# Performance work log

Hardware: AMD Instinct MI355X
Metric: run time of the kernel (lower is better)

## Reference

```python
import jax, jax.numpy as jnp
import numpy as np

HEAD, D_MODEL, D_KV = 16, 1024, 64
B, NQ, NK = 2, 2048, 2048


def setup_inputs() -> dict:
    key = jax.random.key(0)
    ks = jax.random.split(key, 10)
    s = 1.0 / np.sqrt(D_MODEL)
    return {
        "queries": jax.random.normal(ks[0], (B, NQ, D_MODEL), jnp.float32),
        "keys": jax.random.normal(ks[1], (B, NK, D_MODEL), jnp.float32),
        "values": jax.random.normal(ks[2], (B, NK, D_MODEL), jnp.float32),
        "group_prob": jax.random.uniform(ks[3], (B, 1, NQ, NK), jnp.float32),
        "attention_mask": jnp.ones((B, NK), jnp.int32),
        "Wq": jax.random.normal(ks[4], (D_MODEL, HEAD * D_KV), jnp.float32) * s,
        "bq": jnp.zeros((HEAD * D_KV,), jnp.float32),
        "Wk": jax.random.normal(ks[5], (D_MODEL, HEAD * D_KV), jnp.float32) * s,
        "bk": jnp.zeros((HEAD * D_KV,), jnp.float32),
        "Wv": jax.random.normal(ks[6], (D_MODEL, HEAD * D_KV), jnp.float32) * s,
        "bv": jnp.zeros((HEAD * D_KV,), jnp.float32),
    }


def reference(queries, keys, values, group_prob, attention_mask, Wq, bq, Wk, bk, Wv, bv):
    b_s, nq, _ = queries.shape
    nk = keys.shape[1]
    # projections -> [b, h, n, d]
    q = (queries @ Wq + bq).reshape(b_s, nq, HEAD, D_KV).transpose(0, 2, 1, 3)
    k = (keys @ Wk + bk).reshape(b_s, nk, HEAD, D_KV).transpose(0, 2, 1, 3)
    v = (values @ Wv + bv).reshape(b_s, nk, HEAD, D_KV).transpose(0, 2, 1, 3)
    att = jnp.einsum("bhqd,bhkd->bhqk", q, k) / np.sqrt(D_KV).astype(np.float32)
    # NOTE: original uses non-in-place `att.masked_fill(...)` and discards the
    # result, so attention_mask has NO effect on the computation. Replicated.
    att = jax.nn.softmax(att, axis=-1)
    att = att * group_prob  # post-softmax group gating, broadcast over heads
    out = jnp.einsum("bhqk,bhkd->bhqd", att, v)
    return out.transpose(0, 2, 1, 3).reshape(b_s, nq, D_MODEL)
```

## Files before the change

kernel.cpp:

```cpp
#include <hip/hip_runtime.h>
#include <hip/hip_bf16.h>
#include <cstdint>

typedef unsigned short ushort_t;
typedef __attribute__((ext_vector_type(8))) short short8;
typedef __attribute__((ext_vector_type(4))) short short4v;
typedef __attribute__((ext_vector_type(4))) float floatx4;
typedef __attribute__((ext_vector_type(4))) unsigned int uintx4;
typedef __attribute__((ext_vector_type(4))) unsigned short ushort4_t;

#define H_   16
#define DKV_ 64
#define DM_  1024
#define B_   2
#define NQ_  2048
#define NK_  2048

__device__ __forceinline__ unsigned short f2bf(float f) {
  union { float f; unsigned int u; } v; v.f = f;
  unsigned int u = v.u;
  return (unsigned short)((u + 0x7fffu + ((u >> 16) & 1u)) >> 16);
}

__device__ __forceinline__ float fexp2(float x) { return __builtin_amdgcn_exp2f(x); }
__device__ __forceinline__ float frcp(float x)  { return __builtin_amdgcn_rcpf(x); }

__device__ __forceinline__ unsigned int cvt_pk_bf16(float lo, float hi) {
  unsigned int r;
  asm("v_cvt_pk_bf16_f32 %0, %1, %2" : "=v"(r) : "v"(lo), "v"(hi));
  return r;
}

__device__ __forceinline__ floatx4 mfma16(short8 a, short8 b, floatx4 c) {
  return __builtin_amdgcn_mfma_f32_16x16x32_bf16(a, b, c, 0, 0, 0);
}

__device__ __forceinline__ void gload_lds16(const ushort_t* g, ushort_t* l) {
  __builtin_amdgcn_global_load_lds(
      (const __attribute__((address_space(1))) void*)g,
      (__attribute__((address_space(3))) void*)l, 16, 0, 0);
}

__global__ __launch_bounds__(256) void cast_x_kernel(
    const float* __restrict__ q, const float* __restrict__ k,
    const float* __restrict__ v, ushort_t* __restrict__ dst)
{
  const int t = blockIdx.y;
  const float* src = (t == 0) ? q : (t == 1) ? k : v;
  ushort_t* d = dst + (size_t)t * 4096 * 1024;
  const int gid = blockIdx.x * 256 + threadIdx.x;
  #pragma unroll
  for (int u = 0; u < 8; u++) {
    const int i4 = u * 131072 + gid;
    floatx4 f = ((const floatx4*)src)[i4];
    ushort4_t o;
    #pragma unroll
    for (int e = 0; e < 4; e++) o[e] = f2bf(f[e]);
    *(ushort4_t*)&d[(size_t)i4 * 4] = o;
  }
}

__global__ __launch_bounds__(256) void cast_wt_kernel(
    const float* __restrict__ Wq, const float* __restrict__ Wk,
    const float* __restrict__ Wv, ushort_t* __restrict__ WtAll)
{
  __shared__ ushort_t tile[32][33];
  const int t = blockIdx.z;
  const float* W = (t == 0) ? Wq : (t == 1) ? Wk : Wv;
  ushort_t* Wt = WtAll + (size_t)t * 1024 * 1024;
  const int n0 = blockIdx.x * 32, k0 = blockIdx.y * 32;
  const int tid = threadIdx.x, r = tid >> 3, c4 = (tid & 7) * 4;
  floatx4 f = *(const floatx4*)&W[(size_t)(k0 + r) * 1024 + n0 + c4];
  #pragma unroll
  for (int e = 0; e < 4; e++) tile[r][c4 + e] = f2bf(f[e]);
  __syncthreads();
  ushort4_t o;
  #pragma unroll
  for (int e = 0; e < 4; e++) o[e] = tile[c4 + e][r];
  *(ushort4_t*)&Wt[(size_t)(n0 + r) * 1024 + k0 + c4] = o;
}

__global__ __launch_bounds__(256, 2) void proj_kernel2(
    const ushort_t* __restrict__ Xbf, const ushort_t* __restrict__ WtAll,
    const float* __restrict__ bq, const float* __restrict__ bk,
    const float* __restrict__ bv,
    ushort_t* __restrict__ Qb, ushort_t* __restrict__ Kb, ushort_t* __restrict__ Vt)
{
  const int mode = blockIdx.z;
  const ushort_t* X  = Xbf  + (size_t)mode * 4096 * 1024;
  const ushort_t* Wt = WtAll + (size_t)mode * 1024 * 1024;
  const float* bias  = (mode == 0) ? bq : (mode == 1) ? bk : bv;
  ushort_t* dst      = (mode == 0) ? Qb : (mode == 1) ? Kb : Vt;

  __shared__ ushort_t SM[8192];
  ushort_t* SA = SM;
  ushort_t* SB = SM + 4096;

  const int tid = threadIdx.x, lane = tid & 63, wid = tid >> 6;
  const int c = lane & 15, g = lane >> 4;
  const int m0 = blockIdx.y * 128, n0 = blockIdx.x * 128;
  const int wm = wid & 1, wn = wid >> 1, mb = wm * 64, nb = wn * 64;
  const int srow = lane >> 2;
  const int schunk = (lane & 3) * 8;

  floatx4 acc[4][4];
  #pragma unroll
  for (int i = 0; i < 4; i++)
    #pragma unroll
    for (int j = 0; j < 4; j++) acc[i][j] = floatx4{0.f, 0.f, 0.f, 0.f};

  for (int k0 = 0; k0 < DM_; k0 += 32) {
    __syncthreads();
    #pragma unroll
    for (int u = 0; u < 2; u++) {
      const int t = wid * 2 + u;
      gload_lds16(&X [(size_t)(m0 + t * 16 + srow) * 1024 + k0 + schunk], &SA[t * 512]);
      gload_lds16(&Wt[(size_t)(n0 + t * 16 + srow) * 1024 + k0 + schunk], &SB[t * 512]);
    }
    __syncthreads();

    short8 af[4], bfr[4];
    #pragma unroll
    for (int i = 0; i < 4; i++) af[i]  = *(const short8*)&SA[(mb + i * 16 + c) * 32 + g * 8];
    #pragma unroll
    for (int j = 0; j < 4; j++) bfr[j] = *(const short8*)&SB[(nb + j * 16 + c) * 32 + g * 8];
    #pragma unroll
    for (int i = 0; i < 4; i++)
      #pragma unroll
      for (int j = 0; j < 4; j++) acc[i][j] = mfma16(af[i], bfr[j], acc[i][j]);
  }

  __syncthreads();
  const float scale = (mode == 0) ? 0.18033688011112042f : 1.0f;
  ushort_t* EP = SM + wid * 2048;
  const int hh = (n0 + nb) >> 6;

  if (mode != 2) {
    for (int jj = 0; jj < 2; jj++) {
      #pragma unroll
      for (int jt = 0; jt < 2; jt++) {
        const int j = jj * 2 + jt;
        const float bb = bias[n0 + nb + j * 16 + c];
        #pragma unroll
        for (int i = 0; i < 4; i++)
          #pragma unroll
          for (int r = 0; r < 4; r++)
            EP[(i * 16 + g * 4 + r) * 32 + jt * 16 + c] =
                f2bf((acc[i][j][r] + bb) * scale);
      }
      #pragma unroll
      for (int u = 0; u < 8; u++) {
        const int rowl = u * 8 + (lane >> 3);
        ushort4_t vv = *(ushort4_t*)&EP[rowl * 32 + (lane & 7) * 4];
        const int rowg = m0 + mb + rowl;
        const int bb2 = rowg >> 11, nn = rowg & 2047;
        *(ushort4_t*)&dst[((size_t)(bb2 * H_ + hh) * NQ_ + nn) * DKV_ +
                          jj * 32 + (lane & 7) * 4] = vv;
      }
    }
  } else {
    const int bb2 = (m0 + mb) >> 11, nloc = (m0 + mb) & 2047;
    for (int j = 0; j < 4; j++) {
      const float bb = bias[n0 + nb + j * 16 + c];
      #pragma unroll
      for (int i = 0; i < 4; i++) {
        ushort4_t pk;
        #pragma unroll
        for (int r = 0; r < 4; r++) pk[r] = f2bf(acc[i][j][r] + bb);
        *(ushort4_t*)&EP[c * 72 + i * 16 + g * 4] = pk;
      }
      const int d0 = j * 16;
      #pragma unroll
      for (int u = 0; u < 2; u++) {
        const int coll = u * 8 + (lane >> 3);
        short8 vv = *(const short8*)&EP[coll * 72 + (lane & 7) * 8];
        *(short8*)&dst[((size_t)(bb2 * H_ + hh) * DKV_ + d0 + coll) * NK_ +
                       nloc + (lane & 7) * 8] = vv;
      }
    }
  }
}

constexpr int LDT = 40;
__global__ __launch_bounds__(256, 2) void proj_kernel_fb(
    const float* __restrict__ Xq, const float* __restrict__ Xk, const float* __restrict__ Xv,
    const float* __restrict__ Wq, const float* __restrict__ Wk, const float* __restrict__ Wv,
    const float* __restrict__ bq, const float* __restrict__ bk, const float* __restrict__ bv,
    ushort_t* __restrict__ Qb, ushort_t* __restrict__ Kb, ushort_t* __restrict__ Vt)
{
  const int mode = blockIdx.z;
  const float* X    = (mode == 0) ? Xq : (mode == 1) ? Xk : Xv;
  const float* W    = (mode == 0) ? Wq : (mode == 1) ? Wk : Wv;
  const float* bias = (mode == 0) ? bq : (mode == 1) ? bk : bv;
  ushort_t* dst     = (mode == 0) ? Qb : (mode == 1) ? Kb : Vt;

  __shared__ ushort_t Asm[128 * LDT];
  __shared__ ushort_t Bsm[128 * LDT];

  const int tid = threadIdx.x, lane = tid & 63, wid = tid >> 6;
  const int m0 = blockIdx.y * 128, n0 = blockIdx.x * 128;
  const int c = lane & 15, g = lane >> 4;
  const int wm = wid & 1, wn = wid >> 1, mb = wm * 64, nb = wn * 64;

  floatx4 acc[4][4];
  #pragma unroll
  for (int i = 0; i < 4; i++)
    #pragma unroll
    for (int j = 0; j < 4; j++) acc[i][j] = floatx4{0.f, 0.f, 0.f, 0.f};

  const int ar = tid >> 1, ah = tid & 1;
  const int bn = tid & 127, bh2 = tid >> 7;

  for (int k0 = 0; k0 < DM_; k0 += 32) {
    const floatx4* ap = (const floatx4*)(X + (size_t)(m0 + ar) * DM_ + k0 + ah * 16);
    floatx4 av0 = ap[0], av1 = ap[1], av2 = ap[2], av3 = ap[3];
    const float* wp = W + (size_t)(k0 + bh2 * 16) * 1024 + n0 + bn;
    float wv[16];
    #pragma unroll
    for (int j = 0; j < 16; j++) wv[j] = wp[j * 1024];
    short8 pa0, pa1, pb0, pb1;
    #pragma unroll
    for (int j = 0; j < 4; j++) {
      pa0[j] = (short)f2bf(av0[j]); pa0[4 + j] = (short)f2bf(av1[j]);
      pa1[j] = (short)f2bf(av2[j]); pa1[4 + j] = (short)f2bf(av3[j]);
    }
    #pragma unroll
    for (int j = 0; j < 8; j++) { pb0[j] = (short)f2bf(wv[j]); pb1[j] = (short)f2bf(wv[8 + j]); }
    __syncthreads();
    *(short8*)&Asm[ar * LDT + ah * 16]      = pa0;
    *(short8*)&Asm[ar * LDT + ah * 16 + 8]  = pa1;
    *(short8*)&Bsm[bn * LDT + bh2 * 16]     = pb0;
    *(short8*)&Bsm[bn * LDT + bh2 * 16 + 8] = pb1;
    __syncthreads();
    short8 af[4], bfr[4];
    #pragma unroll
    for (int i = 0; i < 4; i++) af[i]  = *(const short8*)&Asm[(mb + i * 16 + c) * LDT + g * 8];
    #pragma unroll
    for (int j = 0; j < 4; j++) bfr[j] = *(const short8*)&Bsm[(nb + j * 16 + c) * LDT + g * 8];
    #pragma unroll
    for (int i = 0; i < 4; i++)
      #pragma unroll
      for (int j = 0; j < 4; j++) acc[i][j] = mfma16(af[i], bfr[j], acc[i][j]);
  }
  #pragma unroll
  for (int j = 0; j < 4; j++) {
    const int col = n0 + nb + j * 16 + c;
    const float bv_ = bias[col];
    const int h = col >> 6, d = col & 63;
    #pragma unroll
    for (int i = 0; i < 4; i++)
      #pragma unroll
      for (int r = 0; r < 4; r++) {
        const int row = m0 + mb + i * 16 + g * 4 + r;
        const int b = row >> 11, n = row & 2047;
        float v = acc[i][j][r] + bv_;
        if (mode == 0) {
          v *= 0.18033688011112042f;
          dst[((size_t)(b * H_ + h) * NQ_ + n) * DKV_ + d] = f2bf(v);
        } else if (mode == 1) {
          dst[((size_t)(b * H_ + h) * NQ_ + n) * DKV_ + d] = f2bf(v);
        } else {
          dst[((size_t)(b * H_ + h) * DKV_ + d) * NK_ + n] = f2bf(v);
        }
      }
  }
}

__global__ __launch_bounds__(512, 4) void attn_kernel(
    const ushort_t* __restrict__ Qb, const ushort_t* __restrict__ Kb,
    const ushort_t* __restrict__ Vt, const float* __restrict__ gp,
    float* __restrict__ out)
{
  __shared__ ushort_t Ks[2][64 * 72];
  __shared__ ushort_t Vs[2][64 * 72];

  constexpr int NT = NK_ / 64;

  const int tid = threadIdx.x, lane = tid & 63, wid = tid >> 6;
  const int c = lane & 15, g = lane >> 4;
  const int h = blockIdx.x, b = blockIdx.z;
  const int bh = b * H_ + h;
  const int qw = blockIdx.y * 128 + wid * 16;

  const ushort_t* Qp = Qb + (size_t)bh * NQ_ * DKV_;
  const ushort_t* Kp = Kb + (size_t)bh * NK_ * DKV_;
  const ushort_t* Vp = Vt + (size_t)bh * DKV_ * NK_;
  const float* gpq = gp + (size_t)b * NQ_ * NK_ + (size_t)(qw + c) * NK_;

  const int srow = tid >> 3;
  const int u    = tid & 7;
  const int scol = u * 8;
  const int so_lo = 32 * (u >> 2) + 8 * ((2 * u) & 3) + 4 * ((u >> 1) & 1);
  const int so_hi = 32 * (u >> 2) + 8 * ((2 * u + 1) & 3) + 4 * ((u >> 1) & 1);

  short8 qf[2];
  #pragma unroll
  for (int kc = 0; kc < 2; kc++)
    qf[kc] = *(const short8*)&Qp[(qw + c) * DKV_ + kc * 32 + g * 8];

  *(short8*)&Ks[0][srow * 72 + scol] = *(const short8*)&Kp[(size_t)srow * DKV_ + scol];
  {
    short8 v8 = *(const short8*)&Vp[(size_t)srow * NK_ + scol];
    short4v vl, vh;
    #pragma unroll
    for (int e = 0; e < 4; e++) { vl[e] = v8[e]; vh[e] = v8[4 + e]; }
    *(short4v*)&Vs[0][srow * 72 + so_lo] = vl;
    *(short4v*)&Vs[0][srow * 72 + so_hi] = vh;
  }
  short8 kA = *(const short8*)&Kp[(size_t)(64 + srow) * DKV_ + scol];
  short8 vA = *(const short8*)&Vp[(size_t)srow * NK_ + 64 + scol];
  short8 kB = {}, vB = {};
  floatx4 gpA[4], gpB[4];
  #pragma unroll
  for (int jk = 0; jk < 4; jk++)
    gpA[jk] = *(const floatx4*)&gpq[jk * 16 + g * 4];
  __syncthreads();

  floatx4 o[4];
  float l = 0.f;
  #pragma unroll
  for (int jd = 0; jd < 4; jd++) o[jd] = floatx4{0.f, 0.f, 0.f, 0.f};

#define ATTN_BODY(T, CUR, GPC, GPN, KA, VA, KB, VB)                          \
  {                                                                          \
    const int t_ = (T);                                                      \
            \
    if (t_ + 2 < NT) {                                                       \
      const int k2 = (t_ + 2) * 64;                                          \
      KB = *(const short8*)&Kp[(size_t)(k2 + srow) * DKV_ + scol];           \
      VB = *(const short8*)&Vp[(size_t)srow * NK_ + k2 + scol];              \
    }                                                                        \
                                     \
    if (t_ + 1 < NT) {                                                       \
      const int k1 = (t_ + 1) * 64;                                          \
      _Pragma("unroll")                                                      \
      for (int jk = 0; jk < 4; jk++)                                         \
        GPN[jk] = *(const floatx4*)&gpq[k1 + jk * 16 + g * 4];               \
    }                                                                        \
                  \
    floatx4 s_[4];                                                           \
    _Pragma("unroll")                                                        \
    for (int jk = 0; jk < 4; jk++) {                                         \
      s_[jk] = floatx4{0.f, 0.f, 0.f, 0.f};                                  \
      _Pragma("unroll")                                                      \
      for (int kc = 0; kc < 2; kc++) {                                       \
        short8 kf = *(const short8*)&Ks[CUR][(jk * 16 + c) * 72 + kc * 32 + g * 8]; \
        s_[jk] = mfma16(kf, qf[kc], s_[jk]);                                 \
      }                                                                      \
    }                                                                        \
              \
    uintx4 afw_[2];                                                          \
    _Pragma("unroll")                                                        \
    for (int jk = 0; jk < 4; jk++) {                                         \
      const float p0 = fexp2(s_[jk][0]);                                     \
      const float p1 = fexp2(s_[jk][1]);                                     \
      const float p2 = fexp2(s_[jk][2]);                                     \
      const float p3 = fexp2(s_[jk][3]);                                     \
      l += (p0 + p1) + (p2 + p3);                                            \
      const unsigned int w0 = cvt_pk_bf16(p0 * GPC[jk][0], p1 * GPC[jk][1]); \
      const unsigned int w1 = cvt_pk_bf16(p2 * GPC[jk][2], p3 * GPC[jk][3]); \
      afw_[jk >> 1][2 * (jk & 1) + 0] = w0;                                  \
      afw_[jk >> 1][2 * (jk & 1) + 1] = w1;                                  \
    }                                                                        \
             \
    _Pragma("unroll")                                                        \
    for (int kc = 0; kc < 2; kc++) {                                         \
      const short8 af_ = __builtin_bit_cast(short8, afw_[kc]);               \
      _Pragma("unroll")                                                      \
      for (int jd = 0; jd < 4; jd++) {                                       \
        short8 vf = *(const short8*)&Vs[CUR][(jd * 16 + c) * 72 + kc * 32 + g * 8]; \
        o[jd] = mfma16(af_, vf, o[jd]);                                      \
      }                                                                      \
    }                                                                        \
              \
    if (t_ + 1 < NT) {                                                       \
      *(short8*)&Ks[(CUR) ^ 1][srow * 72 + scol] = KA;                       \
      short4v vl_, vh_;                                                      \
      _Pragma("unroll")                                                      \
      for (int e = 0; e < 4; e++) { vl_[e] = VA[e]; vh_[e] = VA[4 + e]; }    \
      *(short4v*)&Vs[(CUR) ^ 1][srow * 72 + so_lo] = vl_;                    \
      *(short4v*)&Vs[(CUR) ^ 1][srow * 72 + so_hi] = vh_;                    \
    }                                                                        \
    __syncthreads();                                                         \
  }

  for (int tt = 0; tt < NT; tt += 2) {
    ATTN_BODY(tt,     0, gpA, gpB, kA, vA, kB, vB)
    ATTN_BODY(tt + 1, 1, gpB, gpA, kB, vB, kA, vA)
  }
#undef ATTN_BODY

  float lf = l;
  lf += __shfl_xor(lf, 16);
  lf += __shfl_xor(lf, 32);
  const float inv = frcp(lf);
  float invr[4];
  #pragma unroll
  for (int r = 0; r < 4; r++) invr[r] = __shfl(inv, g * 4 + r);

  #pragma unroll
  for (int jd = 0; jd < 4; jd++)
    #pragma unroll
    for (int r = 0; r < 4; r++) {
      const int row = qw + g * 4 + r;
      out[(size_t)(b * NQ_ + row) * 1024 + h * 64 + jd * 16 + c] =
          o[jd][r] * invr[r];
    }
}

extern "C" void kernel_launch(void* const* d_in, const int* in_sizes, int n_in,
                              void* d_out, int out_size, void* d_ws, size_t ws_size,
                              hipStream_t stream) {
  const float* queries = (const float*)d_in[0];
  const float* keys    = (const float*)d_in[1];
  const float* values  = (const float*)d_in[2];
  const float* gp      = (const float*)d_in[3];
  const float* Wq = (const float*)d_in[5];
  const float* bq = (const float*)d_in[6];
  const float* Wk = (const float*)d_in[7];
  const float* bk = (const float*)d_in[8];
  const float* Wv = (const float*)d_in[9];
  const float* bv = (const float*)d_in[10];

  const size_t SZ_QKV = (size_t)3 * B_ * H_ * NQ_ * DKV_;
  const size_t SZ_X   = (size_t)3 * 4096 * 1024;
  const size_t SZ_W   = (size_t)3 * 1024 * 1024;
  const size_t NEED   = (SZ_QKV + SZ_X + SZ_W) * sizeof(ushort_t);

  ushort_t* Qb = (ushort_t*)d_ws;
  ushort_t* Kb = Qb + (size_t)B_ * H_ * NQ_ * DKV_;
  ushort_t* Vt = Kb + (size_t)B_ * H_ * NK_ * DKV_;
  float* out = (float*)d_out;

  if (ws_size >= NEED) {
    ushort_t* Xbf = Qb + SZ_QKV;
    ushort_t* Wt  = Xbf + SZ_X;
    cast_x_kernel<<<dim3(512, 3), 256, 0, stream>>>(queries, keys, values, Xbf);
    cast_wt_kernel<<<dim3(32, 32, 3), 256, 0, stream>>>(Wq, Wk, Wv, Wt);
    proj_kernel2<<<dim3(8, 32, 3), 256, 0, stream>>>(
        Xbf, Wt, bq, bk, bv, Qb, Kb, Vt);
  } else {
    proj_kernel_fb<<<dim3(8, 32, 3), 256, 0, stream>>>(
        queries, keys, values, Wq, Wk, Wv, bq, bk, bv, Qb, Kb, Vt);
  }
  attn_kernel<<<dim3(H_, NQ_ / 128, B_), 512, 0, stream>>>(Qb, Kb, Vt, gp, out);
}
```

Baseline: 256.2 us.

## Read K/V fragments directly from global memory, drop LDS staging and barriers

The attention kernel no longer stages K and V tiles through shared memory with double buffering and __syncthreads. Each wave instead loads its MFMA fragments straight from global memory, relying on L2/cache reuse across the waves of a block. The projection kernels now write V in the pre-permuted column order the attention loop expects. The change also remaps block indices so heads sharing an XCD are grouped, and adds s_setprio around the MFMA sections. This removes LDS traffic and barrier stalls, but adds global-load latency and redundant loads across waves that must be hidden by occupancy.

```diff
diff --git a/kernel.cpp b/kernel.cpp
--- a/kernel.cpp
+++ b/kernel.cpp
@@ -160,6 +160,9 @@
     }
   } else {
     const int bb2 = (m0 + mb) >> 11, nloc = (m0 + mb) & 2047;
+    const int u2 = lane & 7;
+    const int slo = 32 * (u2 >> 2) + 8 * ((2 * u2) & 3) + 4 * ((u2 >> 1) & 1);
+    const int shi = 32 * (u2 >> 2) + 8 * ((2 * u2 + 1) & 3) + 4 * ((u2 >> 1) & 1);
     for (int j = 0; j < 4; j++) {
       const float bb = bias[n0 + nb + j * 16 + c];
       #pragma unroll
@@ -173,9 +176,13 @@
       #pragma unroll
       for (int u = 0; u < 2; u++) {
         const int coll = u * 8 + (lane >> 3);
-        short8 vv = *(const short8*)&EP[coll * 72 + (lane & 7) * 8];
-        *(short8*)&dst[((size_t)(bb2 * H_ + hh) * DKV_ + d0 + coll) * NK_ +
-                       nloc + (lane & 7) * 8] = vv;
+        short8 vv = *(const short8*)&EP[coll * 72 + u2 * 8];
+        short4v vl, vh;
+        #pragma unroll
+        for (int e = 0; e < 4; e++) { vl[e] = vv[e]; vh[e] = vv[4 + e]; }
+        ushort_t* base = &dst[((size_t)(bb2 * H_ + hh) * DKV_ + d0 + coll) * NK_ + nloc];
+        *(short4v*)&base[slo] = vl;
+        *(short4v*)&base[shi] = vh;
       }
     }
   }
@@ -260,7 +267,11 @@
         } else if (mode == 1) {
           dst[((size_t)(b * H_ + h) * NQ_ + n) * DKV_ + d] = f2bf(v);
         } else {
-          dst[((size_t)(b * H_ + h) * DKV_ + d) * NK_ + n] = f2bf(v);
+          const int tb = n & ~63, w = n & 63, u2 = w >> 3, e = w & 7;
+          const int slo = 32 * (u2 >> 2) + 8 * ((2 * u2) & 3) + 4 * ((u2 >> 1) & 1);
+          const int shi = 32 * (u2 >> 2) + 8 * ((2 * u2 + 1) & 3) + 4 * ((u2 >> 1) & 1);
+          const int phys = tb + (e < 4 ? slo + e : shi + e - 4);
+          dst[((size_t)(b * H_ + h) * DKV_ + d) * NK_ + phys] = f2bf(v);
         }
       }
   }
@@ -271,83 +282,63 @@
     const ushort_t* __restrict__ Vt, const float* __restrict__ gp,
     float* __restrict__ out)
 {
-  __shared__ ushort_t Ks[2][64 * 72];
-  __shared__ ushort_t Vs[2][64 * 72];
-
   constexpr int NT = NK_ / 64;
 
   const int tid = threadIdx.x, lane = tid & 63, wid = tid >> 6;
   const int c = lane & 15, g = lane >> 4;
-  const int h = blockIdx.x, b = blockIdx.z;
-  const int bh = b * H_ + h;
-  const int qw = blockIdx.y * 128 + wid * 16;
+
+  const int flat = blockIdx.x + (blockIdx.y << 4) + (blockIdx.z << 8);
+  const int xcd = flat & 7, i = flat >> 3;
+  const int qy = i & 15;
+  const int bh = xcd + ((i >> 4) << 3);
+  const int b = bh >> 4, h = bh & 15;
+
+  const int qw = qy * 128 + wid * 16;
 
   const ushort_t* Qp = Qb + (size_t)bh * NQ_ * DKV_;
   const ushort_t* Kp = Kb + (size_t)bh * NK_ * DKV_;
   const ushort_t* Vp = Vt + (size_t)bh * DKV_ * NK_;
   const float* gpq = gp + (size_t)b * NQ_ * NK_ + (size_t)(qw + c) * NK_;
 
-  const int srow = tid >> 3;
-  const int u    = tid & 7;
-  const int scol = u * 8;
-  const int so_lo = 32 * (u >> 2) + 8 * ((2 * u) & 3) + 4 * ((u >> 1) & 1);
-  const int so_hi = 32 * (u >> 2) + 8 * ((2 * u + 1) & 3) + 4 * ((u >> 1) & 1);
-
   short8 qf[2];
   #pragma unroll
   for (int kc = 0; kc < 2; kc++)
     qf[kc] = *(const short8*)&Qp[(qw + c) * DKV_ + kc * 32 + g * 8];
 
-  *(short8*)&Ks[0][srow * 72 + scol] = *(const short8*)&Kp[(size_t)srow * DKV_ + scol];
-  {
-    short8 v8 = *(const short8*)&Vp[(size_t)srow * NK_ + scol];
-    short4v vl, vh;
-    #pragma unroll
-    for (int e = 0; e < 4; e++) { vl[e] = v8[e]; vh[e] = v8[4 + e]; }
-    *(short4v*)&Vs[0][srow * 72 + so_lo] = vl;
-    *(short4v*)&Vs[0][srow * 72 + so_hi] = vh;
-  }
-  short8 kA = *(const short8*)&Kp[(size_t)(64 + srow) * DKV_ + scol];
-  short8 vA = *(const short8*)&Vp[(size_t)srow * NK_ + 64 + scol];
-  short8 kB = {}, vB = {};
+  floatx4 o[4];
+  float l = 0.f;
+  #pragma unroll
+  for (int jd = 0; jd < 4; jd++) o[jd] = floatx4{0.f, 0.f, 0.f, 0.f};
+
   floatx4 gpA[4], gpB[4];
   #pragma unroll
   for (int jk = 0; jk < 4; jk++)
     gpA[jk] = *(const floatx4*)&gpq[jk * 16 + g * 4];
-  __syncthreads();
-
-  floatx4 o[4];
-  float l = 0.f;
-  #pragma unroll
-  for (int jd = 0; jd < 4; jd++) o[jd] = floatx4{0.f, 0.f, 0.f, 0.f};
-
-#define ATTN_BODY(T, CUR, GPC, GPN, KA, VA, KB, VB)                          \
+
+#define ATTN_BODY(T, GPC, GPN)                                               \
   {                                                                          \
     const int t_ = (T);                                                      \
-            \
-    if (t_ + 2 < NT) {                                                       \
-      const int k2 = (t_ + 2) * 64;                                          \
-      KB = *(const short8*)&Kp[(size_t)(k2 + srow) * DKV_ + scol];           \
-      VB = *(const short8*)&Vp[(size_t)srow * NK_ + k2 + scol];              \
-    }                                                                        \
-                                     \
+    const int k0 = t_ * 64;                                                  \
     if (t_ + 1 < NT) {                                                       \
-      const int k1 = (t_ + 1) * 64;                                          \
+      const int k1 = k0 + 64;                                                \
       _Pragma("unroll")                                                      \
       for (int jk = 0; jk < 4; jk++)                                         \
         GPN[jk] = *(const floatx4*)&gpq[k1 + jk * 16 + g * 4];               \
     }                                                                        \
                   \
     floatx4 s_[4];                                                           \
+    __builtin_amdgcn_s_setprio(1);                                           \
     _Pragma("unroll")                                                        \
     for (int jk = 0; jk < 4; jk++) {                                         \
       s_[jk] = floatx4{0.f, 0.f, 0.f, 0.f};                                  \
       _Pragma("unroll")                                                      \
       for (int kc = 0; kc < 2; kc++) {                                       \
-        short8 kf = *(const short8*)&Ks[CUR][(jk * 16 + c) * 72 + kc * 32 + g * 8]; \
+        short8 kf = *(const short8*)&Kp[(size_t)(k0 + jk * 16 + c) * DKV_ +  \
+                                        kc * 32 + g * 8];                    \
         s_[jk] = mfma16(kf, qf[kc], s_[jk]);                                 \
       }                                                                      \
     }                                                                        \
+    __builtin_amdgcn_s_setprio(0);                                           \
               \
     uintx4 afw_[2];                                                          \
     _Pragma("unroll")                                                        \
@@ -362,31 +353,24 @@
       afw_[jk >> 1][2 * (jk & 1) + 0] = w0;                                  \
       afw_[jk >> 1][2 * (jk & 1) + 1] = w1;                                  \
     }                                                                        \
-             \
+       \
+    __builtin_amdgcn_s_setprio(1);                                           \
     _Pragma("unroll")                                                        \
     for (int kc = 0; kc < 2; kc++) {                                         \
       const short8 af_ = __builtin_bit_cast(short8, afw_[kc]);               \
       _Pragma("unroll")                                                      \
       for (int jd = 0; jd < 4; jd++) {                                       \
-        short8 vf = *(const short8*)&Vs[CUR][(jd * 16 + c) * 72 + kc * 32 + g * 8]; \
+        short8 vf = *(const short8*)&Vp[(size_t)(jd * 16 + c) * NK_ + k0 +   \
+                                        kc * 32 + g * 8];                    \
         o[jd] = mfma16(af_, vf, o[jd]);                                      \
       }                                                                      \
     }                                                                        \
-              \
-    if (t_ + 1 < NT) {                                                       \
-      *(short8*)&Ks[(CUR) ^ 1][srow * 72 + scol] = KA;                       \
-      short4v vl_, vh_;                                                      \
-      _Pragma("unroll")                                                      \
-      for (int e = 0; e < 4; e++) { vl_[e] = VA[e]; vh_[e] = VA[4 + e]; }    \
-      *(short4v*)&Vs[(CUR) ^ 1][srow * 72 + so_lo] = vl_;                    \
-      *(short4v*)&Vs[(CUR) ^ 1][srow * 72 + so_hi] = vh_;                    \
-    }                                                                        \
-    __syncthreads();                                                         \
+    __builtin_amdgcn_s_setprio(0);                                           \
   }
 
   for (int tt = 0; tt < NT; tt += 2) {
-    ATTN_BODY(tt,     0, gpA, gpB, kA, vA, kB, vB)
-    ATTN_BODY(tt + 1, 1, gpB, gpA, kB, vB, kA, vA)
+    ATTN_BODY(tt,     gpA, gpB)
+    ATTN_BODY(tt + 1, gpB, gpA)
   }
 #undef ATTN_BODY
 
```

After: 451.9 us. 1.76x slower.
